# Kernel optimization log

Hardware: AMD Instinct MI355X
Metric: run time of the kernel (lower is better)

Reference implementation:

```python
import jax, jax.numpy as jnp
import numpy as np

E = 1024
H = 16
DH = E // H
WINDOW = 128
TAU = 0.0
GLOBAL_IDX = np.array([0], dtype=np.int64)


def setup_inputs() -> dict:
    key = jax.random.key(0)
    ks = jax.random.split(key, 10)
    B, L = 2, 2048
    s = 0.02
    return {
        "x": jax.random.normal(ks[0], (B, L, E), dtype=jnp.float32),
        "pos_bias": jax.random.normal(ks[1], (L, L), dtype=jnp.float32),
        "Wq": jax.random.normal(ks[2], (E, E), dtype=jnp.float32) * s,
        "bq": jnp.zeros((E,), dtype=jnp.float32),
        "Wk": jax.random.normal(ks[3], (E, E), dtype=jnp.float32) * s,
        "bk": jnp.zeros((E,), dtype=jnp.float32),
        "Wv": jax.random.normal(ks[4], (E, E), dtype=jnp.float32) * s,
        "bv": jnp.zeros((E,), dtype=jnp.float32),
        "Wo": jax.random.normal(ks[5], (E, E), dtype=jnp.float32) * s,
        "bo": jnp.zeros((E,), dtype=jnp.float32),
    }


def reference(x, pos_bias, Wq, bq, Wk, bk, Wv, bv, Wo, bo):
    B, L, _ = x.shape
    scale = jnp.sqrt(jnp.asarray(DH, dtype=x.dtype))

    def proj(W, b):
        # torch Linear: x @ W.T + b, then [B,L,H,Dh] -> [B,H,L,Dh]
        return (x @ W.T + b).reshape(B, L, H, DH).transpose(0, 2, 1, 3)

    q = proj(Wq, bq)
    k = proj(Wk, bk)
    v = proj(Wv, bv)

    scores = jnp.einsum("bhqd,bhkd->bhqk", q, k) / scale  # [B,H,L,L]

    idx = jnp.arange(L)
    dist = jnp.abs(idx[None, :] - idx[:, None])
    local = dist <= WINDOW
    g = jnp.zeros((L,), dtype=bool).at[jnp.asarray(GLOBAL_IDX)].set(True)
    allowed = local | g[:, None] | g[None, :]  # [L,L]

    neg_inf = jnp.finfo(scores.dtype).min
    gate = scores > TAU
    keep = allowed[None, None] & gate
    scores = jnp.where(keep, scores, neg_inf) + pos_bias[None, None]
    attn = jax.nn.softmax(scores, axis=-1)  # dropout is identity in eval

    out = jnp.einsum("bhqk,bhkd->bhqd", attn, v)
    out = out.transpose(0, 2, 1, 3).reshape(B, L, E)
    return out @ Wo.T + bo
```

## Files before the change

### kernel.cpp

```cpp
#include <hip/hip_runtime.h>
#include <float.h>

#define BB 2
#define LL 2048
#define EE 1024
#define HH 16
#define DHD 64
#define WIN 128

typedef __attribute__((ext_vector_type(8))) short short8v;
typedef __attribute__((ext_vector_type(8))) _Float16 half8v;
typedef __attribute__((ext_vector_type(4))) float f32x4;

static __device__ __forceinline__ unsigned short f2h(float f) {
    union { _Float16 h; unsigned short u; } x; x.h = (_Float16)f; return x.u;
}
static __device__ __forceinline__ float h2f_u(unsigned short u) {
    union { unsigned short u; _Float16 h; } x{u}; return (float)x.h;
}
static __device__ __forceinline__ void f2h_split(float f, unsigned short& hi,
                                                 unsigned short& lo) {
    _Float16 h = (_Float16)f;
    _Float16 l = (_Float16)(f - (float)h);
    union { _Float16 h; unsigned short u; } uh, ul;
    uh.h = h; ul.h = l;
    hi = uh.u;
    lo = ul.u;
}

#define KTL_PER_BH   262144
#define KTL_PER_TILE 2048
#define VTL_PER_BH   131072
#define VTL_PER_TILE 2048

__global__ __launch_bounds__(256) void prep_split(
    const float* __restrict__ x, const float* __restrict__ Wq,
    const float* __restrict__ Wk,
    unsigned short* __restrict__ xh, unsigned short* __restrict__ xl,
    unsigned short* __restrict__ wqh, unsigned short* __restrict__ wql,
    unsigned short* __restrict__ wkh, unsigned short* __restrict__ wkl)
{
    const size_t NX = (size_t)BB * LL * EE;
    const size_t NW = (size_t)EE * EE;
    const size_t total = NX + 2 * NW;
    const size_t stride = (size_t)gridDim.x * 256 * 4;
    for (size_t i = (size_t)(blockIdx.x * 256 + threadIdx.x) * 4;
         i < total; i += stride) {
        const float* src; unsigned short *dh, *dl; size_t off;
        if (i < NX)            { src = x;  dh = xh;  dl = xl;  off = i; }
        else if (i < NX + NW)  { src = Wq; dh = wqh; dl = wql; off = i - NX; }
        else                   { src = Wk; dh = wkh; dl = wkl; off = i - NX - NW; }
        const float4 v = *(const float4*)(src + off);
        ushort4 h4, l4;
        f2h_split(v.x, h4.x, l4.x);
        f2h_split(v.y, h4.y, l4.y);
        f2h_split(v.z, h4.z, l4.z);
        f2h_split(v.w, h4.w, l4.w);
        *(ushort4*)(dh + off) = h4;
        *(ushort4*)(dl + off) = l4;
    }
}

__global__ __launch_bounds__(256) void pack_bias(
    const float* __restrict__ pb, float* __restrict__ pbp,
    float* __restrict__ pb0, const float* __restrict__ Wo,
    unsigned short* __restrict__ woh)
{
    const int r = blockIdx.x;
    int lo_w = (r & ~15) - WIN; if (lo_w < 0) lo_w = 0;
    for (int t = threadIdx.x; t < 272; t += 256) {
        const int c = lo_w + t;
        pbp[(size_t)r * 272 + t] = (c < LL) ? pb[(size_t)r * LL + c] : 0.f;
    }
    if (threadIdx.x == 0) pb0[r] = pb[(size_t)r * LL];
    const size_t i = (size_t)blockIdx.x * 256 + threadIdx.x;
    const float2 v = ((const float2*)Wo)[i];
    ushort2 o2; o2.x = f2h(v.x); o2.y = f2h(v.y);
    ((ushort2*)woh)[i] = o2;
}

__global__ __launch_bounds__(256, 3) void gemm_qkv(
    const unsigned short* __restrict__ xh, const unsigned short* __restrict__ xl,
    const unsigned short* __restrict__ wqh, const unsigned short* __restrict__ wql,
    const unsigned short* __restrict__ wkh, const unsigned short* __restrict__ wkl,
    const float* __restrict__ Wv,
    const float* __restrict__ bq, const float* __restrict__ bk,
    const float* __restrict__ bv,
    unsigned short* __restrict__ qhi, unsigned short* __restrict__ qlo,
    unsigned short* __restrict__ ktl,
    unsigned short* __restrict__ vtl)
{
    __shared__ unsigned short Ah[128 * 40], Al[128 * 40];
    __shared__ unsigned short Bqh[64 * 40], Bql[64 * 40];
    __shared__ unsigned short Bkh[64 * 40], Bkl[64 * 40];

    const int bid = blockIdx.x;
    const bool isqk = bid < 512;
    const int tile = isqk ? bid : bid - 512;
    const int col0 = (tile & 15) * 64;
    const int row0 = (tile >> 4) * 128;
    const int tid = threadIdx.x;
    const int w = tid >> 6, lane = tid & 63;
    const int wr = w >> 1, wc = w & 1;
    const int lr16 = lane & 15, kg = lane >> 4;
    const int arow_i = tid >> 1, ahalf = tid & 1;
    const int sbaseA = arow_i * 40 + ahalf * 16;
    const int brow_i = tid >> 2, bquad = tid & 3;
    const int sbaseB = brow_i * 40 + bquad * 8;

    const unsigned short* arow_h = xh + (size_t)(row0 + arow_i) * EE + ahalf * 16;
    const unsigned short* arow_l = xl + (size_t)(row0 + arow_i) * EE + ahalf * 16;
    const unsigned short* bq_h = wqh + (size_t)(col0 + brow_i) * EE + bquad * 8;
    const unsigned short* bq_l = wql + (size_t)(col0 + brow_i) * EE + bquad * 8;
    const unsigned short* bk_h = wkh + (size_t)(col0 + brow_i) * EE + bquad * 8;
    const unsigned short* bk_l = wkl + (size_t)(col0 + brow_i) * EE + bquad * 8;
    const float* vrow = Wv + (size_t)(col0 + brow_i) * EE + bquad * 8;

    if (isqk) {
        f32x4 accQ[4][2], accK[4][2];
#pragma unroll
        for (int i = 0; i < 4; i++)
#pragma unroll
            for (int j = 0; j < 2; j++) {
                accQ[i][j] = (f32x4){0.f, 0.f, 0.f, 0.f};
                accK[i][j] = (f32x4){0.f, 0.f, 0.f, 0.f};
            }

        for (int t = 0; t < EE / 32; t++) {
            const int k0 = t * 32;
            const short8v ra0 = *(const short8v*)(arow_h + k0);
            const short8v ra1 = *(const short8v*)(arow_h + k0 + 8);
            const short8v la0 = *(const short8v*)(arow_l + k0);
            const short8v la1 = *(const short8v*)(arow_l + k0 + 8);
            const short8v qb = *(const short8v*)(bq_h + k0);
            const short8v ql = *(const short8v*)(bq_l + k0);
            const short8v kb = *(const short8v*)(bk_h + k0);
            const short8v kl = *(const short8v*)(bk_l + k0);
            __syncthreads();
            *(short8v*)&Ah[sbaseA + 0] = ra0;
            *(short8v*)&Ah[sbaseA + 8] = ra1;
            *(short8v*)&Al[sbaseA + 0] = la0;
            *(short8v*)&Al[sbaseA + 8] = la1;
            *(short8v*)&Bqh[sbaseB] = qb;
            *(short8v*)&Bql[sbaseB] = ql;
            *(short8v*)&Bkh[sbaseB] = kb;
            *(short8v*)&Bkl[sbaseB] = kl;
            __syncthreads();

            half8v afh[4], afl[4], bfh[2], bfl[2];
#pragma unroll
            for (int mr = 0; mr < 4; mr++) {
                const int off = (wr * 64 + mr * 16 + lr16) * 40 + kg * 8;
                afh[mr] = *(const half8v*)&Ah[off];
                afl[mr] = *(const half8v*)&Al[off];
            }
#pragma unroll
            for (int nr = 0; nr < 2; nr++) {
                const int off = (wc * 32 + nr * 16 + lr16) * 40 + kg * 8;
                bfh[nr] = *(const half8v*)&Bqh[off];
                bfl[nr] = *(const half8v*)&Bql[off];
            }
#pragma unroll
            for (int mr = 0; mr < 4; mr++)
#pragma unroll
                for (int nr = 0; nr < 2; nr++) {
                    accQ[mr][nr] = __builtin_amdgcn_mfma_f32_16x16x32_f16(
                        afl[mr], bfh[nr], accQ[mr][nr], 0, 0, 0);
                    accQ[mr][nr] = __builtin_amdgcn_mfma_f32_16x16x32_f16(
                        afh[mr], bfl[nr], accQ[mr][nr], 0, 0, 0);
                    accQ[mr][nr] = __builtin_amdgcn_mfma_f32_16x16x32_f16(
                        afh[mr], bfh[nr], accQ[mr][nr], 0, 0, 0);
                }
#pragma unroll
            for (int nr = 0; nr < 2; nr++) {
                const int off = (wc * 32 + nr * 16 + lr16) * 40 + kg * 8;
                bfh[nr] = *(const half8v*)&Bkh[off];
                bfl[nr] = *(const half8v*)&Bkl[off];
            }
#pragma unroll
            for (int mr = 0; mr < 4; mr++)
#pragma unroll
                for (int nr = 0; nr < 2; nr++) {
                    accK[mr][nr] = __builtin_amdgcn_mfma_f32_16x16x32_f16(
                        afl[mr], bfh[nr], accK[mr][nr], 0, 0, 0);
                    accK[mr][nr] = __builtin_amdgcn_mfma_f32_16x16x32_f16(
                        afh[mr], bfl[nr], accK[mr][nr], 0, 0, 0);
                    accK[mr][nr] = __builtin_amdgcn_mfma_f32_16x16x32_f16(
                        afh[mr], bfh[nr], accK[mr][nr], 0, 0, 0);
                }
        }

#pragma unroll
        for (int mr = 0; mr < 4; mr++) {
#pragma unroll
            for (int nr = 0; nr < 2; nr++) {
                const int n = col0 + wc * 32 + nr * 16 + lr16;
                const float bbq = bq[n];
                const float bbk = bk[n];
#pragma unroll
                for (int j = 0; j < 4; j++) {
                    const int m = row0 + wr * 64 + mr * 16 + kg * 4 + j;
                    const int bi = m >> 11, l = m & (LL - 1);
                    const int hh = n >> 6, d = n & 63;
                    const int bhh = bi * HH + hh;
                    const size_t o = ((size_t)bhh * LL + l) * DHD + d;
                    unsigned short hu, lu;
                    f2h_split(accQ[mr][nr][j] + bbq, hu, lu);
                    qhi[o] = hu; qlo[o] = lu;
                    f2h_split(accK[mr][nr][j] + bbk, hu, lu);
                    const size_t ko = (size_t)bhh * KTL_PER_BH +
                                      (size_t)(l >> 4) * KTL_PER_TILE +
                                      (size_t)(d >> 3) * 128 +
                                      (size_t)(l & 15) * 8 + (d & 7);
                    ktl[ko] = hu;
                    ktl[ko + 1024] = lu;
                }
            }
        }
    } else {
        f32x4 acc[4][2];
#pragma unroll
        for (int i = 0; i < 4; i++)
#pragma unroll
            for (int j = 0; j < 2; j++) acc[i][j] = (f32x4){0.f, 0.f, 0.f, 0.f};

        for (int t = 0; t < EE / 32; t++) {
            const int k0 = t * 32;
            const short8v ra0 = *(const short8v*)(arow_h + k0);
            const short8v ra1 = *(const short8v*)(arow_h + k0 + 8);
            const float4 f0 = *(const float4*)(vrow + k0);
            const float4 f1 = *(const float4*)(vrow + k0 + 4);
            unsigned short ub[8];
            ub[0] = f2h(f0.x); ub[1] = f2h(f0.y); ub[2] = f2h(f0.z); ub[3] = f2h(f0.w);
            ub[4] = f2h(f1.x); ub[5] = f2h(f1.y); ub[6] = f2h(f1.z); ub[7] = f2h(f1.w);
            __syncthreads();
            *(short8v*)&Ah[sbaseA + 0] = ra0;
            *(short8v*)&Ah[sbaseA + 8] = ra1;
            *(short8v*)&Bqh[sbaseB] = *(short8v*)&ub[0];
            __syncthreads();

            half8v af[4], bf[2];
#pragma unroll
            for (int mr = 0; mr < 4; mr++)
                af[mr] = *(const half8v*)&Ah[(wr*64 + mr*16 + lr16)*40 + kg*8];
#pragma unroll
            for (int nr = 0; nr < 2; nr++)
                bf[nr] = *(const half8v*)&Bqh[(wc*32 + nr*16 + lr16)*40 + kg*8];
#pragma unroll
            for (int mr = 0; mr < 4; mr++)
#pragma unroll
                for (int nr = 0; nr < 2; nr++)
                    acc[mr][nr] = __builtin_amdgcn_mfma_f32_16x16x32_f16(
                        af[mr], bf[nr], acc[mr][nr], 0, 0, 0);
        }

#pragma unroll
        for (int mr = 0; mr < 4; mr++) {
#pragma unroll
            for (int nr = 0; nr < 2; nr++) {
                const int n = col0 + wc * 32 + nr * 16 + lr16;
                const float bb = bv[n];
#pragma unroll
                for (int j = 0; j < 4; j++) {
                    const int m = row0 + wr * 64 + mr * 16 + kg * 4 + j;
                    const float val = acc[mr][nr][j] + bb;
                    const int bi = m >> 11, l = m & (LL - 1);
                    const int hh = n >> 6, d = n & 63;
                    const size_t vo = (size_t)(bi * HH + hh) * VTL_PER_BH +
                                      (size_t)(l >> 5) * VTL_PER_TILE +
                                      (size_t)d * 32 + (l & 31);
                    vtl[vo] = f2h(val);
                }
            }
        }
    }
}

__global__ __launch_bounds__(256) void attn_mfma(
    const unsigned short* __restrict__ qhi, const unsigned short* __restrict__ qlo,
    const unsigned short* __restrict__ ktl,
    const unsigned short* __restrict__ vtl, const float* __restrict__ pos_bias,
    const float* __restrict__ pbp, const float* __restrict__ pb0,
    unsigned short* __restrict__ attn16)
{
    __shared__ __align__(16) unsigned short Pl[4][16][296];
    __shared__ float s0s[4][16];

    const int bid = blockIdx.x;
    const int tid = threadIdx.x;

    if (bid < 32) {
        const int head = bid;
        const int b = head >> 4, h = head & 15;
        float* sc = (float*)&Pl[0][0][0];
        float* red = sc + LL;
        float* qs = red + 256;
        const size_t bh = (size_t)(b * HH + h);
        const size_t bhL = bh * LL;
        const unsigned short* ktb = ktl + bh * KTL_PER_BH;
        const unsigned short* vtb = vtl + bh * VTL_PER_BH;

        if (tid < DHD)
            qs[tid] = h2f_u(qhi[bhL * DHD + tid]) + h2f_u(qlo[bhL * DHD + tid]);
        __syncthreads();

        for (int j = tid; j < LL; j += 256) {
            const unsigned short* tb = ktb + (size_t)(j >> 4) * KTL_PER_TILE +
                                       (size_t)(j & 15) * 8;
            float s = 0.f;
#pragma unroll
            for (int d8 = 0; d8 < 8; d8++) {
                const half8v kh8 = *(const half8v*)(tb + d8 * 128);
                const half8v kl8 = *(const half8v*)(tb + 1024 + d8 * 128);
#pragma unroll
                for (int e = 0; e < 8; e++)
                    s = fmaf(qs[d8 * 8 + e], (float)kh8[e] + (float)kl8[e], s);
            }
            s *= 0.125f;
            sc[j] = (s > 0.f) ? s + pos_bias[j] : -FLT_MAX;
        }
        __syncthreads();

        float m = -FLT_MAX;
        for (int j = tid; j < LL; j += 256) m = fmaxf(m, sc[j]);
        red[tid] = m;
        __syncthreads();
        for (int s = 128; s > 0; s >>= 1) {
            if (tid < s) red[tid] = fmaxf(red[tid], red[tid + s]);
            __syncthreads();
        }
        m = red[0];
        __syncthreads();

        float lsum = 0.f;
        for (int j = tid; j < LL; j += 256) {
            const float p = expf(sc[j] - m);
            sc[j] = p;
            lsum += p;
        }
        red[tid] = lsum;
        __syncthreads();
        for (int s = 128; s > 0; s >>= 1) {
            if (tid < s) red[tid] += red[tid + s];
            __syncthreads();
        }
        const float inv = 1.0f / red[0];
        __syncthreads();

        const int d = tid & 63, part = tid >> 6;
        float a = 0.f;
        for (int j0 = part * 8; j0 < LL; j0 += 32) {
            const half8v v8 = *(const half8v*)(vtb +
                (size_t)(j0 >> 5) * VTL_PER_TILE + (size_t)d * 32 + (j0 & 31));
#pragma unroll
            for (int e = 0; e < 8; e++)
                a = fmaf(sc[j0 + e], (float)v8[e], a);
        }
        red[tid] = a;
        __syncthreads();
        if (tid < 64) {
            const float tot = (red[tid] + red[tid + 64]) +
                              (red[tid + 128] + red[tid + 192]);
            attn16[(size_t)b * LL * EE + h * DHD + tid] = f2h(tot * inv);
        }
        return;
    }

    const int vbid = bid - 32;
    const int head = vbid & 31, chunk = vbid >> 5;
    const int b = head >> 4, h = head & 15;
    const int w = tid >> 6, lane = tid & 63;
    const int lq = lane & 15, kg = lane >> 4;
    const int r0w = chunk * 64 + w * 16;

    const size_t bh = (size_t)(b * HH + h);
    const size_t bhL = bh * LL;
    const unsigned short* qhb = qhi + (bhL + r0w) * DHD;
    const unsigned short* qlb = qlo + (bhL + r0w) * DHD;
    const unsigned short* ktb = ktl + bh * KTL_PER_BH;
    const unsigned short* vtb = vtl + bh * VTL_PER_BH;

    int lo = r0w - WIN; if (lo < 0) lo = 0;
    int hi = r0w + 15 + WIN; if (hi > LL - 1) hi = LL - 1;
    const bool has0 = (lo > 0);
    const int t0 = lo >> 4;

    for (int idx = lane; idx < 96; idx += 64) {
        const int rr = idx / 6, cc = 272 + (idx % 6) * 4;
        *(unsigned long long*)&Pl[w][rr][cc] = 0ull;
    }

    half8v qfh[2], qfl[2];
#pragma unroll
    for (int kf = 0; kf < 2; kf++) {
        const int off = lq * DHD + kf * 32 + kg * 8;
        qfh[kf] = *(const half8v*)(qhb + off);
        qfl[kf] = *(const half8v*)(qlb + off);
    }

    f32x4 acc[17];
#pragma unroll
    for (int f = 0; f < 17; f++) {
        int tt = t0 + f;
        if (tt > 127) tt = 127;
        const unsigned short* tb = ktb + (size_t)tt * KTL_PER_TILE;
        const int lofs = kg * 128 + lq * 8;
        const half8v b0h = *(const half8v*)(tb + lofs);
        const half8v b1h = *(const half8v*)(tb + 512 + lofs);
        const half8v b0l = *(const half8v*)(tb + 1024 + lofs);
        const half8v b1l = *(const half8v*)(tb + 1536 + lofs);
        f32x4 a = (f32x4){0.f, 0.f, 0.f, 0.f};
        a = __builtin_amdgcn_mfma_f32_16x16x32_f16(qfl[0], b0h, a, 0, 0, 0);
        a = __builtin_amdgcn_mfma_f32_16x16x32_f16(qfh[0], b0l, a, 0, 0, 0);
        a = __builtin_amdgcn_mfma_f32_16x16x32_f16(qfh[0], b0h, a, 0, 0, 0);
        a = __builtin_amdgcn_mfma_f32_16x16x32_f16(qfl[1], b1h, a, 0, 0, 0);
        a = __builtin_amdgcn_mfma_f32_16x16x32_f16(qfh[1], b1l, a, 0, 0, 0);
        a = __builtin_amdgcn_mfma_f32_16x16x32_f16(qfh[1], b1h, a, 0, 0, 0);
        acc[f] = a;
    }

    float sc0 = -FLT_MAX;
    if (has0) {
        float part = 0.f;
        const int rowoff = lq * DHD;
#pragma unroll
        for (int e = 0; e < 16; e++) {
            const int d = kg * 16 + e;
            const float qv = h2f_u(qhb[rowoff + d]) + h2f_u(qlb[rowoff + d]);
            const int kofs = (d >> 3) * 128 + (d & 7);
            const float kv = h2f_u(ktb[kofs]) + h2f_u(ktb[1024 + kofs]);
            part = fmaf(qv, kv, part);
        }
        part += __shfl_xor(part, 16);
        part += __shfl_xor(part, 32);
        const float s = part * 0.125f;
        sc0 = (s > 0.f) ? s + pb0[r0w + lq] : -FLT_MAX;
    }
    if (lane < 16) s0s[w][lq] = sc0;

#pragma unroll
    for (int f = 0; f < 17; f++) {
        const int c = lo + f * 16 + lq;
        const bool cok = (c <= hi);
        f32x4 s4 = acc[f];
#pragma unroll
        for (int rg = 0; rg < 4; rg++) {
            const int r = r0w + kg * 4 + rg;
            const bool allowed = cok &&
                ((c == 0) || ((c >= r - WIN) && (c <= r + WIN)));
            const float s = s4[rg] * 0.125f;
            float sc = -FLT_MAX;
            if (allowed && s > 0.f)
                sc = s + pbp[(size_t)r * 272 + f * 16 + lq];
            s4[rg] = sc;
        }
        acc[f] = s4;
    }

    float s0r[4], mx[4];
#pragma unroll
    for (int rg = 0; rg < 4; rg++) {
        s0r[rg] = s0s[w][kg * 4 + rg];
        float m = s0r[rg];
#pragma unroll
        for (int f = 0; f < 17; f++) m = fmaxf(m, acc[f][rg]);
        m = fmaxf(m, __shfl_xor(m, 1));
        m = fmaxf(m, __shfl_xor(m, 2));
        m = fmaxf(m, __shfl_xor(m, 4));
        m = fmaxf(m, __shfl_xor(m, 8));
        mx[rg] = m;
    }

    float sum0 = 0.f, sum1 = 0.f, sum2 = 0.f, sum3 = 0.f;
#pragma unroll
    for (int f = 0; f < 17; f++) {
        const float p0_ = __expf(acc[f][0] - mx[0]); sum0 += p0_;
        const float p1_ = __expf(acc[f][1] - mx[1]); sum1 += p1_;
        const float p2_ = __expf(acc[f][2] - mx[2]); sum2 += p2_;
        const float p3_ = __expf(acc[f][3] - mx[3]); sum3 += p3_;
        Pl[w][kg * 4 + 0][f * 16 + lq] = f2h(p0_);
        Pl[w][kg * 4 + 1][f * 16 + lq] = f2h(p1_);
        Pl[w][kg * 4 + 2][f * 16 + lq] = f2h(p2_);
        Pl[w][kg * 4 + 3][f * 16 + lq] = f2h(p3_);
    }

    float inv[4], p0v[4];
    float sums[4] = {sum0, sum1, sum2, sum3};
#pragma unroll
    for (int rg = 0; rg < 4; rg++) {
        float s = sums[rg];
        s += __shfl_xor(s, 1);
        s += __shfl_xor(s, 2);
        s += __shfl_xor(s, 4);
        s += __shfl_xor(s, 8);
        const float p0 = has0 ? __expf(s0r[rg] - mx[rg]) : 0.f;
        p0v[rg] = p0;
        inv[rg] = 1.0f / (s + p0);
    }

    f32x4 pacc[4];
#pragma unroll
    for (int nf = 0; nf < 4; nf++) pacc[nf] = (f32x4){0.f, 0.f, 0.f, 0.f};
#pragma unroll
    for (int kf = 0; kf < 9; kf++) {
        const half8v pa = *(const half8v*)&Pl[w][lq][kf * 32 + kg * 8];
        int c0 = lo + kf * 32 + kg * 8;
        if (c0 > LL - 8) c0 = LL - 8;
        const size_t vbase = (size_t)(c0 >> 5) * VTL_PER_TILE + (c0 & 31);
#pragma unroll
        for (int nf = 0; nf < 4; nf++) {
            const half8v vb =
                *(const half8v*)(vtb + vbase + (size_t)(nf * 16 + lq) * 32);
            pacc[nf] = __builtin_amdgcn_mfma_f32_16x16x32_f16(
                pa, vb, pacc[nf], 0, 0, 0);
        }
    }

#pragma unroll
    for (int nf = 0; nf < 4; nf++) {
        const int n = nf * 16 + lq;
        const float v0 = has0 ? h2f_u(vtb[(size_t)n * 32]) : 0.f;
#pragma unroll
        for (int rg = 0; rg < 4; rg++) {
            const int r = r0w + kg * 4 + rg;
            const float o = (pacc[nf][rg] + p0v[rg] * v0) * inv[rg];
            if (r != 0)
                attn16[((size_t)(b * LL + r)) * EE + h * DHD + n] = f2h(o);
        }
    }
}

__global__ __launch_bounds__(256) void gemm_o(
    const unsigned short* __restrict__ attn16, const unsigned short* __restrict__ woh,
    const float* __restrict__ bo, float* __restrict__ out)
{
    __shared__ unsigned short Ah[128 * 40], Bh[128 * 40];

    const int tid = threadIdx.x;
    const int w = tid >> 6, lane = tid & 63;
    const int wr = w >> 1, wc = w & 1;
    const int lr16 = lane & 15, kg = lane >> 4;
    const int row0 = blockIdx.y * 128, col0 = blockIdx.x * 128;
    const int srow = tid >> 1, shalf = tid & 1;
    const int sbase = srow * 40 + shalf * 16;

    const unsigned short* arow = attn16 + (size_t)(row0 + srow) * EE + shalf * 16;
    const unsigned short* brow = woh + (size_t)(col0 + srow) * EE + shalf * 16;

    f32x4 acc[4][4];
#pragma unroll
    for (int i = 0; i < 4; i++)
#pragma unroll
        for (int j = 0; j < 4; j++) acc[i][j] = (f32x4){0.f, 0.f, 0.f, 0.f};

    short8v ra0 = *(const short8v*)(arow + 0);
    short8v ra1 = *(const short8v*)(arow + 8);
    short8v rb0 = *(const short8v*)(brow + 0);
    short8v rb1 = *(const short8v*)(brow + 8);

    for (int t = 0; t < EE / 32; t++) {
        __syncthreads();
        *(short8v*)&Ah[sbase + 0] = ra0;
        *(short8v*)&Ah[sbase + 8] = ra1;
        *(short8v*)&Bh[sbase + 0] = rb0;
        *(short8v*)&Bh[sbase + 8] = rb1;
        __syncthreads();

        if (t + 1 < EE / 32) {
            const int k0 = (t + 1) * 32;
            ra0 = *(const short8v*)(arow + k0);
            ra1 = *(const short8v*)(arow + k0 + 8);
            rb0 = *(const short8v*)(brow + k0);
            rb1 = *(const short8v*)(brow + k0 + 8);
        }

        half8v af[4], bf[4];
#pragma unroll
        for (int mr = 0; mr < 4; mr++)
            af[mr] = *(const half8v*)&Ah[(wr*64 + mr*16 + lr16)*40 + kg*8];
#pragma unroll
        for (int nr = 0; nr < 4; nr++)
            bf[nr] = *(const half8v*)&Bh[(wc*64 + nr*16 + lr16)*40 + kg*8];
#pragma unroll
        for (int mr = 0; mr < 4; mr++)
#pragma unroll
            for (int nr = 0; nr < 4; nr++)
                acc[mr][nr] = __builtin_amdgcn_mfma_f32_16x16x32_f16(
                    af[mr], bf[nr], acc[mr][nr], 0, 0, 0);
    }

#pragma unroll
    for (int mr = 0; mr < 4; mr++) {
#pragma unroll
        for (int nr = 0; nr < 4; nr++) {
            const int n = col0 + wc * 64 + nr * 16 + lr16;
            const float bb = bo[n];
#pragma unroll
            for (int j = 0; j < 4; j++) {
                const int m = row0 + wr * 64 + mr * 16 + kg * 4 + j;
                out[(size_t)m * EE + n] = acc[mr][nr][j] + bb;
            }
        }
    }
}

extern "C" void kernel_launch(void* const* d_in, const int* in_sizes, int n_in,
                              void* d_out, int out_size, void* d_ws, size_t ws_size,
                              hipStream_t stream) {
    const float* x        = (const float*)d_in[0];
    const float* pos_bias = (const float*)d_in[1];
    const float* Wq = (const float*)d_in[2];
    const float* bq = (const float*)d_in[3];
    const float* Wk = (const float*)d_in[4];
    const float* bk = (const float*)d_in[5];
    const float* Wv = (const float*)d_in[6];
    const float* bv = (const float*)d_in[7];
    const float* Wo = (const float*)d_in[8];
    const float* bo = (const float*)d_in[9];
    float* out = (float*)d_out;

    const size_t M1 = (size_t)1024 * 1024;
    unsigned short* u = (unsigned short*)d_ws;
    unsigned short* xh  = u;
    unsigned short* xl  = u + 4 * M1;
    unsigned short* wqh = u + 8 * M1;
    unsigned short* wql = u + 9 * M1;
    unsigned short* wkh = u + 10 * M1;
    unsigned short* wkl = u + 11 * M1;
    unsigned short* qhi = u + 12 * M1;
    unsigned short* qlo = u + 16 * M1;
    unsigned short* ktl = u + 20 * M1;
    unsigned short* vtl = u + 28 * M1;
    unsigned short* attn16 = xh;
    float* pbp = (float*)(u + 4 * M1);
    float* pb0 = pbp + (size_t)2048 * 272;
    unsigned short* woh = u + 7 * M1;

    prep_split<<<dim3(2048), 256, 0, stream>>>(x, Wq, Wk, xh, xl,
                                               wqh, wql, wkh, wkl);
    gemm_qkv<<<dim3(1024), 256, 0, stream>>>(xh, xl, wqh, wql, wkh, wkl,
                                             Wv, bq, bk, bv,
                                             qhi, qlo, ktl, vtl);
    pack_bias<<<dim3(2048), 256, 0, stream>>>(pos_bias, pbp, pb0, Wo, woh);
    attn_mfma<<<dim3(1056), 256, 0, stream>>>(qhi, qlo, ktl, vtl,
                                              pos_bias, pbp, pb0, attn16);
    gemm_o<<<dim3(8, 32), 256, 0, stream>>>(attn16, woh, bo, out);
}
```

Measured before the change: 189.0 us.

## Fuse Q, K, V projections into uniform 64x64 tile blocks

Replaces the split grid, where some blocks computed fused Q/K on 128x64 tiles and others computed V alone, with a single block type. Each block computes Q, K and V for one 64x64 output tile, sharing the loaded x tile across all three. This is meant to remove the load imbalance between heavy QK blocks and light V blocks and to avoid reloading x for V. In exchange, tiles are smaller, so weight reuse per block drops, and the block count and per-block register use change.

```diff
diff --git a/kernel.cpp b/kernel.cpp
--- a/kernel.cpp
+++ b/kernel.cpp
@@ -90,187 +90,145 @@
     unsigned short* __restrict__ ktl,
     unsigned short* __restrict__ vtl)
 {
-    __shared__ unsigned short Ah[128 * 40], Al[128 * 40];
+    __shared__ unsigned short Ah[64 * 40], Al[64 * 40];
     __shared__ unsigned short Bqh[64 * 40], Bql[64 * 40];
     __shared__ unsigned short Bkh[64 * 40], Bkl[64 * 40];
+    __shared__ unsigned short Bvh[64 * 40];
 
     const int bid = blockIdx.x;
-    const bool isqk = bid < 512;
-    const int tile = isqk ? bid : bid - 512;
-    const int col0 = (tile & 15) * 64;
-    const int row0 = (tile >> 4) * 128;
+    const int col0 = (bid & 15) * 64;
+    const int row0 = (bid >> 4) * 64;
     const int tid = threadIdx.x;
     const int w = tid >> 6, lane = tid & 63;
     const int wr = w >> 1, wc = w & 1;
     const int lr16 = lane & 15, kg = lane >> 4;
-    const int arow_i = tid >> 1, ahalf = tid & 1;
-    const int sbaseA = arow_i * 40 + ahalf * 16;
-    const int brow_i = tid >> 2, bquad = tid & 3;
-    const int sbaseB = brow_i * 40 + bquad * 8;
-
-    const unsigned short* arow_h = xh + (size_t)(row0 + arow_i) * EE + ahalf * 16;
-    const unsigned short* arow_l = xl + (size_t)(row0 + arow_i) * EE + ahalf * 16;
-    const unsigned short* bq_h = wqh + (size_t)(col0 + brow_i) * EE + bquad * 8;
-    const unsigned short* bq_l = wql + (size_t)(col0 + brow_i) * EE + bquad * 8;
-    const unsigned short* bk_h = wkh + (size_t)(col0 + brow_i) * EE + bquad * 8;
-    const unsigned short* bk_l = wkl + (size_t)(col0 + brow_i) * EE + bquad * 8;
-    const float* vrow = Wv + (size_t)(col0 + brow_i) * EE + bquad * 8;
-
-    if (isqk) {
-        f32x4 accQ[4][2], accK[4][2];
-#pragma unroll
-        for (int i = 0; i < 4; i++)
-#pragma unroll
-            for (int j = 0; j < 2; j++) {
-                accQ[i][j] = (f32x4){0.f, 0.f, 0.f, 0.f};
-                accK[i][j] = (f32x4){0.f, 0.f, 0.f, 0.f};
+    const int ri = tid >> 2, rq = tid & 3;
+    const int sbase = ri * 40 + rq * 8;
+
+    const unsigned short* arow_h = xh + (size_t)(row0 + ri) * EE + rq * 8;
+    const unsigned short* arow_l = xl + (size_t)(row0 + ri) * EE + rq * 8;
+    const unsigned short* bq_h = wqh + (size_t)(col0 + ri) * EE + rq * 8;
+    const unsigned short* bq_l = wql + (size_t)(col0 + ri) * EE + rq * 8;
+    const unsigned short* bk_h = wkh + (size_t)(col0 + ri) * EE + rq * 8;
+    const unsigned short* bk_l = wkl + (size_t)(col0 + ri) * EE + rq * 8;
+    const float* vrow = Wv + (size_t)(col0 + ri) * EE + rq * 8;
+
+    f32x4 accQ[2][2], accK[2][2], accV[2][2];
+#pragma unroll
+    for (int i = 0; i < 2; i++)
+#pragma unroll
+        for (int j = 0; j < 2; j++) {
+            accQ[i][j] = (f32x4){0.f, 0.f, 0.f, 0.f};
+            accK[i][j] = (f32x4){0.f, 0.f, 0.f, 0.f};
+            accV[i][j] = (f32x4){0.f, 0.f, 0.f, 0.f};
+        }
+
+    for (int t = 0; t < EE / 32; t++) {
+        const int k0 = t * 32;
+        const short8v ra = *(const short8v*)(arow_h + k0);
+        const short8v la = *(const short8v*)(arow_l + k0);
+        const short8v qb = *(const short8v*)(bq_h + k0);
+        const short8v ql = *(const short8v*)(bq_l + k0);
+        const short8v kb = *(const short8v*)(bk_h + k0);
+        const short8v kl = *(const short8v*)(bk_l + k0);
+        const float4 f0 = *(const float4*)(vrow + k0);
+        const float4 f1 = *(const float4*)(vrow + k0 + 4);
+        unsigned short ub[8];
+        ub[0] = f2h(f0.x); ub[1] = f2h(f0.y); ub[2] = f2h(f0.z); ub[3] = f2h(f0.w);
+        ub[4] = f2h(f1.x); ub[5] = f2h(f1.y); ub[6] = f2h(f1.z); ub[7] = f2h(f1.w);
+        __syncthreads();
+        *(short8v*)&Ah[sbase]  = ra;
+        *(short8v*)&Al[sbase]  = la;
+        *(short8v*)&Bqh[sbase] = qb;
+        *(short8v*)&Bql[sbase] = ql;
+        *(short8v*)&Bkh[sbase] = kb;
+        *(short8v*)&Bkl[sbase] = kl;
+        *(short8v*)&Bvh[sbase] = *(short8v*)&ub[0];
+        __syncthreads();
+
+        half8v afh[2], afl[2], bfh[2], bfl[2];
+#pragma unroll
+        for (int mr = 0; mr < 2; mr++) {
+            const int off = (wr * 32 + mr * 16 + lr16) * 40 + kg * 8;
+            afh[mr] = *(const half8v*)&Ah[off];
+            afl[mr] = *(const half8v*)&Al[off];
+        }
+#pragma unroll
+        for (int nr = 0; nr < 2; nr++) {
+            const int off = (wc * 32 + nr * 16 + lr16) * 40 + kg * 8;
+            bfh[nr] = *(const half8v*)&Bqh[off];
+            bfl[nr] = *(const half8v*)&Bql[off];
+        }
+#pragma unroll
+        for (int mr = 0; mr < 2; mr++)
+#pragma unroll
+            for (int nr = 0; nr < 2; nr++) {
+                accQ[mr][nr] = __builtin_amdgcn_mfma_f32_16x16x32_f16(
+                    afl[mr], bfh[nr], accQ[mr][nr], 0, 0, 0);
+                accQ[mr][nr] = __builtin_amdgcn_mfma_f32_16x16x32_f16(
+                    afh[mr], bfl[nr], accQ[mr][nr], 0, 0, 0);
+                accQ[mr][nr] = __builtin_amdgcn_mfma_f32_16x16x32_f16(
+                    afh[mr], bfh[nr], accQ[mr][nr], 0, 0, 0);
             }
-
-        for (int t = 0; t < EE / 32; t++) {
-            const int k0 = t * 32;
-            const short8v ra0 = *(const short8v*)(arow_h + k0);
-            const short8v ra1 = *(const short8v*)(arow_h + k0 + 8);
-            const short8v la0 = *(const short8v*)(arow_l + k0);
-            const short8v la1 = *(const short8v*)(arow_l + k0 + 8);
-            const short8v qb = *(const short8v*)(bq_h + k0);
-            const short8v ql = *(const short8v*)(bq_l + k0);
-            const short8v kb = *(const short8v*)(bk_h + k0);
-            const short8v kl = *(const short8v*)(bk_l + k0);
-            __syncthreads();
-            *(short8v*)&Ah[sbaseA + 0] = ra0;
-            *(short8v*)&Ah[sbaseA + 8] = ra1;
-            *(short8v*)&Al[sbaseA + 0] = la0;
-            *(short8v*)&Al[sbaseA + 8] = la1;
-            *(short8v*)&Bqh[sbaseB] = qb;
-            *(short8v*)&Bql[sbaseB] = ql;
-            *(short8v*)&Bkh[sbaseB] = kb;
-            *(short8v*)&Bkl[sbaseB] = kl;
-            __syncthreads();
-
-            half8v afh[4], afl[4], bfh[2], bfl[2];
-#pragma unroll
-            for (int mr = 0; mr < 4; mr++) {
-                const int off = (wr * 64 + mr * 16 + lr16) * 40 + kg * 8;
-                afh[mr] = *(const half8v*)&Ah[off];
-                afl[mr] = *(const half8v*)&Al[off];
+#pragma unroll
+        for (int nr = 0; nr < 2; nr++) {
+            const int off = (wc * 32 + nr * 16 + lr16) * 40 + kg * 8;
+            bfh[nr] = *(const half8v*)&Bkh[off];
+            bfl[nr] = *(const half8v*)&Bkl[off];
+        }
+#pragma unroll
+        for (int mr = 0; mr < 2; mr++)
+#pragma unroll
+            for (int nr = 0; nr < 2; nr++) {
+                accK[mr][nr] = __builtin_amdgcn_mfma_f32_16x16x32_f16(
+                    afl[mr], bfh[nr], accK[mr][nr], 0, 0, 0);
+                accK[mr][nr] = __builtin_amdgcn_mfma_f32_16x16x32_f16(
+                    afh[mr], bfl[nr], accK[mr][nr], 0, 0, 0);
+                accK[mr][nr] = __builtin_amdgcn_mfma_f32_16x16x32_f16(
+                    afh[mr], bfh[nr], accK[mr][nr], 0, 0, 0);
             }
 #pragma unroll
-            for (int nr = 0; nr < 2; nr++) {
-                const int off = (wc * 32 + nr * 16 + lr16) * 40 + kg * 8;
-                bfh[nr] = *(const half8v*)&Bqh[off];
-                bfl[nr] = *(const half8v*)&Bql[off];
-            }
-#pragma unroll
-            for (int mr = 0; mr < 4; mr++)
-#pragma unroll
-                for (int nr = 0; nr < 2; nr++) {
-                    accQ[mr][nr] = __builtin_amdgcn_mfma_f32_16x16x32_f16(
-                        afl[mr], bfh[nr], accQ[mr][nr], 0, 0, 0);
-                    accQ[mr][nr] = __builtin_amdgcn_mfma_f32_16x16x32_f16(
-                        afh[mr], bfl[nr], accQ[mr][nr], 0, 0, 0);
-                    accQ[mr][nr] = __builtin_amdgcn_mfma_f32_16x16x32_f16(
-                        afh[mr], bfh[nr], accQ[mr][nr], 0, 0, 0);
-                }
-#pragma unroll
-            for (int nr = 0; nr < 2; nr++) {
-                const int off = (wc * 32 + nr * 16 + lr16) * 40 + kg * 8;
-                bfh[nr] = *(const half8v*)&Bkh[off];
-                bfl[nr] = *(const half8v*)&Bkl[off];
-            }
-#pragma unroll
-            for (int mr = 0; mr < 4; mr++)
-#pragma unroll
-                for (int nr = 0; nr < 2; nr++) {
-                    accK[mr][nr] = __builtin_amdgcn_mfma_f32_16x16x32_f16(
-                        afl[mr], bfh[nr], accK[mr][nr], 0, 0, 0);
-                    accK[mr][nr] = __builtin_amdgcn_mfma_f32_16x16x32_f16(
-                        afh[mr], bfl[nr], accK[mr][nr], 0, 0, 0);
-                    accK[mr][nr] = __builtin_amdgcn_mfma_f32_16x16x32_f16(
-                        afh[mr], bfh[nr], accK[mr][nr], 0, 0, 0);
-                }
-        }
-
-#pragma unroll
-        for (int mr = 0; mr < 4; mr++) {
-#pragma unroll
-            for (int nr = 0; nr < 2; nr++) {
-                const int n = col0 + wc * 32 + nr * 16 + lr16;
-                const float bbq = bq[n];
-                const float bbk = bk[n];
-#pragma unroll
-                for (int j = 0; j < 4; j++) {
-                    const int m = row0 + wr * 64 + mr * 16 + kg * 4 + j;
-                    const int bi = m >> 11, l = m & (LL - 1);
-                    const int hh = n >> 6, d = n & 63;
-                    const int bhh = bi * HH + hh;
-                    const size_t o = ((size_t)bhh * LL + l) * DHD + d;
-                    unsigned short hu, lu;
-                    f2h_split(accQ[mr][nr][j] + bbq, hu, lu);
-                    qhi[o] = hu; qlo[o] = lu;
-                    f2h_split(accK[mr][nr][j] + bbk, hu, lu);
-                    const size_t ko = (size_t)bhh * KTL_PER_BH +
-                                      (size_t)(l >> 4) * KTL_PER_TILE +
-                                      (size_t)(d >> 3) * 128 +
-                                      (size_t)(l & 15) * 8 + (d & 7);
-                    ktl[ko] = hu;
-                    ktl[ko + 1024] = lu;
-                }
-            }
-        }
-    } else {
-        f32x4 acc[4][2];
-#pragma unroll
-        for (int i = 0; i < 4; i++)
-#pragma unroll
-            for (int j = 0; j < 2; j++) acc[i][j] = (f32x4){0.f, 0.f, 0.f, 0.f};
-
-        for (int t = 0; t < EE / 32; t++) {
-            const int k0 = t * 32;
-            const short8v ra0 = *(const short8v*)(arow_h + k0);
-            const short8v ra1 = *(const short8v*)(arow_h + k0 + 8);
-            const float4 f0 = *(const float4*)(vrow + k0);
-            const float4 f1 = *(const float4*)(vrow + k0 + 4);
-            unsigned short ub[8];
-            ub[0] = f2h(f0.x); ub[1] = f2h(f0.y); ub[2] = f2h(f0.z); ub[3] = f2h(f0.w);
-            ub[4] = f2h(f1.x); ub[5] = f2h(f1.y); ub[6] = f2h(f1.z); ub[7] = f2h(f1.w);
-            __syncthreads();
-            *(short8v*)&Ah[sbaseA + 0] = ra0;
-            *(short8v*)&Ah[sbaseA + 8] = ra1;
-            *(short8v*)&Bqh[sbaseB] = *(short8v*)&ub[0];
-            __syncthreads();
-
-            half8v af[4], bf[2];
-#pragma unroll
-            for (int mr = 0; mr < 4; mr++)
-                af[mr] = *(const half8v*)&Ah[(wr*64 + mr*16 + lr16)*40 + kg*8];
+        for (int nr = 0; nr < 2; nr++) {
+            const int off = (wc * 32 + nr * 16 + lr16) * 40 + kg * 8;
+            bfh[nr] = *(const half8v*)&Bvh[off];
+        }
+#pragma unroll
+        for (int mr = 0; mr < 2; mr++)
 #pragma unroll
             for (int nr = 0; nr < 2; nr++)
-                bf[nr] = *(const half8v*)&Bqh[(wc*32 + nr*16 + lr16)*40 + kg*8];
-#pragma unroll
-            for (int mr = 0; mr < 4; mr++)
-#pragma unroll
-                for (int nr = 0; nr < 2; nr++)
-                    acc[mr][nr] = __builtin_amdgcn_mfma_f32_16x16x32_f16(
-                        af[mr], bf[nr], acc[mr][nr], 0, 0, 0);
-        }
-
-#pragma unroll
-        for (int mr = 0; mr < 4; mr++) {
-#pragma unroll
-            for (int nr = 0; nr < 2; nr++) {
-                const int n = col0 + wc * 32 + nr * 16 + lr16;
-                const float bb = bv[n];
-#pragma unroll
-                for (int j = 0; j < 4; j++) {
-                    const int m = row0 + wr * 64 + mr * 16 + kg * 4 + j;
-                    const float val = acc[mr][nr][j] + bb;
-                    const int bi = m >> 11, l = m & (LL - 1);
-                    const int hh = n >> 6, d = n & 63;
-                    const size_t vo = (size_t)(bi * HH + hh) * VTL_PER_BH +
-                                      (size_t)(l >> 5) * VTL_PER_TILE +
-                                      (size_t)d * 32 + (l & 31);
-                    vtl[vo] = f2h(val);
-                }
+                accV[mr][nr] = __builtin_amdgcn_mfma_f32_16x16x32_f16(
+                    afh[mr], bfh[nr], accV[mr][nr], 0, 0, 0);
+    }
+
+#pragma unroll
+    for (int mr = 0; mr < 2; mr++) {
+#pragma unroll
+        for (int nr = 0; nr < 2; nr++) {
+            const int n = col0 + wc * 32 + nr * 16 + lr16;
+            const float bbq = bq[n];
+            const float bbk = bk[n];
+            const float bbv = bv[n];
+#pragma unroll
+            for (int j = 0; j < 4; j++) {
+                const int m = row0 + wr * 32 + mr * 16 + kg * 4 + j;
+                const int bi = m >> 11, l = m & (LL - 1);
+                const int hh = n >> 6, d = n & 63;
+                const int bhh = bi * HH + hh;
+                const size_t o = ((size_t)bhh * LL + l) * DHD + d;
+                unsigned short hu, lu;
+                f2h_split(accQ[mr][nr][j] + bbq, hu, lu);
+                qhi[o] = hu; qlo[o] = lu;
+                f2h_split(accK[mr][nr][j] + bbk, hu, lu);
+                const size_t ko = (size_t)bhh * KTL_PER_BH +
+                                  (size_t)(l >> 4) * KTL_PER_TILE +
+                                  (size_t)(d >> 3) * 128 +
+                                  (size_t)(l & 15) * 8 + (d & 7);
+                ktl[ko] = hu;
+                ktl[ko + 1024] = lu;
+                const size_t vo = (size_t)bhh * VTL_PER_BH +
+                                  (size_t)(l >> 5) * VTL_PER_TILE +
+                                  (size_t)d * 32 + (l & 31);
+                vtl[vo] = f2h(accV[mr][nr][j] + bbv);
             }
         }
     }
```

Measured after the change: 195.9 us. 3.6% more time.
